# Kernel tuning notes

Hardware: AMD Instinct MI355X
Metric: run time of the kernel (lower is better)

The kernel has to match this reference:

```python
import jax, jax.numpy as jnp
import numpy as np

B, F, D, C, K = 131072, 32, 16, 64, 8  # batch, features, qsvt degree, classes, KAN grid
CLIP = 1.0 - 1e-6


def setup_inputs() -> dict:
    key = jax.random.key(0)
    ks = jax.random.split(key, 7)
    return {
        "X": jax.random.normal(ks[0], (B, F), jnp.float32),
        "qsvt_phases": 0.1 * jax.random.normal(ks[1], (D,), jnp.float32),
        "lcu_weights": jax.random.uniform(ks[2], (F, D), jnp.float32),
        "sum_scale": jnp.ones((F,), jnp.float32) + 0.1 * jax.random.normal(ks[3], (F,), jnp.float32),
        "sum_bias": 0.1 * jax.random.normal(ks[4], (F,), jnp.float32),
        "kan_coeff": jax.random.normal(ks[5], (C, F, K), jnp.float32) / np.sqrt(F * K),
        "kan_bias": jnp.zeros((C,), jnp.float32),
    }


def reference(X, qsvt_phases, lcu_weights, sum_scale, sum_bias, kan_coeff, kan_bias):
    # QSVT: Chebyshev-with-phases polynomial features of each scalar input,
    # vectorized over (batch, feature) instead of the original Python loops.
    degree = qsvt_phases.shape[0]
    grid = kan_coeff.shape[-1]
    theta = jnp.arccos(jnp.clip(X, -CLIP, CLIP))                  # [B,F]
    kd = jnp.arange(1, degree + 1, dtype=X.dtype)                 # [D]
    qsvt_vecs = jnp.cos(theta[..., None] * kd + qsvt_phases)      # [B,F,D]
    # LCU block: normalized linear combination over the degree axis -> scalar per (b,f)
    lcu = jnp.sum(qsvt_vecs * lcu_weights, axis=-1) / (
        jnp.sum(jnp.abs(lcu_weights), axis=-1) + 1e-6)            # [B,F]
    # QuantumSumBlock (one per feature): per-feature affine + tanh squash
    feat = jnp.tanh(sum_scale * lcu + sum_bias)                   # [B,F]
    # KAN layer: Chebyshev basis expansion then per-(class,feature,basis) coefficients
    t2 = jnp.arccos(jnp.clip(feat, -CLIP, CLIP))                  # [B,F]
    kk = jnp.arange(grid, dtype=X.dtype)                          # [K]
    basis = jnp.cos(t2[..., None] * kk)                           # [B,F,K]
    return jnp.einsum('bfk,cfk->bc', basis, kan_coeff) + kan_bias  # [B,C]
```

## Files before the change

kernel.cpp:

```cpp
#include <hip/hip_runtime.h>
#include <hip/hip_bf16.h>

#define F 32
#define Dd 16
#define C 64
#define Kk 8
#define CLIPV (1.0f - 1e-6f)
#define K2 2.8853900817779268f
#define NBLK 1024
#define MT 2

typedef short v8s __attribute__((ext_vector_type(8)));
typedef float v4f __attribute__((ext_vector_type(4)));
typedef float v2f __attribute__((ext_vector_type(2)));

static __device__ inline unsigned pkbf(float lo, float hi) {
    const unsigned l = __bfloat16_as_ushort(__float2bfloat16(lo));
    const unsigned hh = __bfloat16_as_ushort(__float2bfloat16(hi));
    return l | (hh << 16);
}

#define BAR_WRITES() do {                                        \
    asm volatile("s_waitcnt lgkmcnt(0)" ::: "memory");           \
    __builtin_amdgcn_s_barrier();                                \
    asm volatile("" ::: "memory");                               \
} while (0)
#define BAR_READS() do {                                         \
    asm volatile("" ::: "memory");                               \
    __builtin_amdgcn_s_barrier();                                \
    asm volatile("" ::: "memory");                               \
} while (0)

__global__ __launch_bounds__(256, 4) void qkan_kernel(
    const float* __restrict__ X,
    const float* __restrict__ phases,
    const float* __restrict__ lcu_w,
    const float* __restrict__ sscale,
    const float* __restrict__ sbias,
    const float* __restrict__ coeff,
    const float* __restrict__ kbias,
    float* __restrict__ out)
{
    __shared__ unsigned short s_basis[F * 512];

    const int tid = threadIdx.x;
    const int lane = tid & 63;
    const int wu = __builtin_amdgcn_readfirstlane(tid >> 6);
    const int h = lane >> 4;
    const int r16 = lane & 15;
    const int fe = tid & 31;
    const int fe7 = fe & 7;
    const int rg = tid >> 5;

    const int rb0 = blockIdx.x * (MT * 64);

    float xq[8];
    {
        const float* xp = X + (size_t)(rb0 + rg * 8) * F + fe;
#pragma unroll
        for (int m = 0; m < 8; ++m) xq[m] = xp[m * F];
    }

    v2f cc[16];
    float fbias;
    {
        const float* lwf = lcu_w + fe * Dd;
        float wv[16];
        float asum = 0.f;
#pragma unroll
        for (int d = 0; d < Dd; ++d) {
            wv[d] = lwf[d];
            asum += fabsf(wv[d]);
        }
        const float sc = K2 * sscale[fe] / (asum + 1e-6f);
#pragma unroll
        for (int d = 0; d < Dd; ++d) {
            float sp, cp;
            __sincosf(phases[d], &sp, &cp);
            cc[d][0] = sc * wv[d] * cp;
            cc[d][1] = -sc * wv[d] * sp;
        }
        fbias = K2 * sbias[fe];
    }

    v8s Bfr[8];
    const int cidx = wu * 16 + r16;
#pragma unroll
    for (int q = 0; q < 8; ++q) {
        const float* gp = coeff + ((size_t)(cidx * F + 4 * q + h) * Kk);
        const float4 g0 = *reinterpret_cast<const float4*>(gp);
        const float4 g1 = *reinterpret_cast<const float4*>(gp + 4);
        union { unsigned u[4]; v8s v; } bb;
        bb.u[0] = pkbf(g0.x, g0.y);
        bb.u[1] = pkbf(g0.z, g0.w);
        bb.u[2] = pkbf(g1.x, g1.y);
        bb.u[3] = pkbf(g1.z, g1.w);
        Bfr[q] = bb.v;
    }
    const float biasreg = kbias[cidx];

    for (int mt = 0; mt < MT; ++mt) {
        const int row_base = rb0 + mt * 64;
        if (mt) BAR_READS();

        float xn[8];
        if (mt + 1 < MT) {
            const float* xp = X + (size_t)(row_base + 64 + rg * 8) * F + fe;
#pragma unroll
            for (int m = 0; m < 8; ++m) xn[m] = xp[m * F];
        }

#pragma unroll
        for (int m = 0; m < 8; ++m) {
            const float x = __builtin_amdgcn_fmed3f(xq[m], -CLIPV, CLIPV);
            const float s1 = __builtin_amdgcn_sqrtf(__builtin_fmaf(-x, x, 1.f));
            const float tx = x + x;
            const v2f tx2 = {tx, tx};
            v2f w = {0.f, 0.f}, wp = {0.f, 0.f};
#pragma unroll
            for (int j = 15; j >= 0; --j) {
                const v2f wn = __builtin_elementwise_fma(tx2, w, cc[j] - wp);
                wp = w;
                w = wn;
            }
            float z = fbias - wp[0];
            z = __builtin_fmaf(x, w[0], z);
            z = __builtin_fmaf(s1, w[1], z);
            const float e = __builtin_amdgcn_exp2f(z);
            const float rr = __builtin_amdgcn_rcpf(e + 1.f);
            const float t = __builtin_fmaf(-2.f, rr, 1.f);
            const float t2 = t + t;
            const float b1 = t;
            const float b2 = t2 * b1 - 1.f;
            const float b3 = t2 * b2 - b1;
            const float b4 = t2 * b3 - b2;
            const float b5 = t2 * b4 - b3;
            const float b6 = t2 * b5 - b4;
            const float b7 = t2 * b6 - b5;
            uint4 pk;
            pk.x = pkbf(1.f, b1);
            pk.y = pkbf(b2, b3);
            pk.z = pkbf(b4, b5);
            pk.w = pkbf(b6, b7);
            *reinterpret_cast<uint4*>(
                &s_basis[fe * 512 + rg * 64 + ((m ^ fe7) << 3)]) = pk;
        }
        BAR_WRITES();

#pragma unroll
        for (int t = 0; t < 4; ++t) {
            const int s0 = ((t * 16 + r16) ^ h) << 3;
            v4f acc = {biasreg, biasreg, biasreg, biasreg};
#pragma unroll
            for (int q = 0; q < 8; ++q) {
                const int idx = (4 * q + h) * 512 + (s0 ^ ((q & 1) << 5));
                const v8s a = *reinterpret_cast<const v8s*>(&s_basis[idx]);
                acc = __builtin_amdgcn_mfma_f32_16x16x32_bf16(a, Bfr[q], acc, 0, 0, 0);
            }
            const int row0 = row_base + t * 16 + h * 4;
#pragma unroll
            for (int i = 0; i < 4; ++i) {
                out[(size_t)(row0 + i) * C + cidx] = acc[i];
            }
        }

        if (mt + 1 < MT) {
#pragma unroll
            for (int m = 0; m < 8; ++m) xq[m] = xn[m];
        }
    }
}

extern "C" void kernel_launch(void* const* d_in, const int* in_sizes, int n_in,
                              void* d_out, int out_size, void* d_ws, size_t ws_size,
                              hipStream_t stream) {
    const float* X  = (const float*)d_in[0];
    const float* ph = (const float*)d_in[1];
    const float* lw = (const float*)d_in[2];
    const float* ss = (const float*)d_in[3];
    const float* sb = (const float*)d_in[4];
    const float* kc = (const float*)d_in[5];
    const float* kb = (const float*)d_in[6];
    float* out = (float*)d_out;
    qkan_kernel<<<dim3(NBLK), dim3(256), 0, stream>>>(X, ph, lw, ss, sb, kc, kb, out);
}
```

Baseline: 25.84 us.

## Switch KAN matmul to 32x32x16 MFMA with per-wave row/column tiling

Replaces the per-wave 16x16x32 bf16 MFMA loop, where each wave covered 16 classes over all 64 rows in four tiles, with 32x32x16 MFMA. Each wave now owns a 32-row by 32-class tile and loads 16 coefficient fragments instead of 8. The intent is fewer MFMA issues and LDS reads per output element and better operand reuse. In exchange it uses more registers for B fragments and accumulators, and drops the occupancy hint in launch_bounds, which may lower occupancy.

```diff
diff --git a/kernel.cpp b/kernel.cpp
--- a/kernel.cpp
+++ b/kernel.cpp
@@ -11,7 +11,7 @@
 #define MT 2
 
 typedef short v8s __attribute__((ext_vector_type(8)));
-typedef float v4f __attribute__((ext_vector_type(4)));
+typedef float v16f __attribute__((ext_vector_type(16)));
 typedef float v2f __attribute__((ext_vector_type(2)));
 
 static __device__ inline unsigned pkbf(float lo, float hi) {
@@ -31,7 +31,7 @@
     asm volatile("" ::: "memory");                               \
 } while (0)
 
-__global__ __launch_bounds__(256, 4) void qkan_kernel(
+__global__ __launch_bounds__(256) void qkan_kernel(
     const float* __restrict__ X,
     const float* __restrict__ phases,
     const float* __restrict__ lcu_w,
@@ -46,11 +46,14 @@
     const int tid = threadIdx.x;
     const int lane = tid & 63;
     const int wu = __builtin_amdgcn_readfirstlane(tid >> 6);
-    const int h = lane >> 4;
-    const int r16 = lane & 15;
+    const int hh = lane >> 5;
+    const int l31 = lane & 31;
     const int fe = tid & 31;
     const int fe7 = fe & 7;
     const int rg = tid >> 5;
+
+    const int rh = wu >> 1;
+    const int ct = wu & 1;
 
     const int rb0 = blockIdx.x * (MT * 64);
 
@@ -83,11 +86,11 @@
         fbias = K2 * sbias[fe];
     }
 
-    v8s Bfr[8];
-    const int cidx = wu * 16 + r16;
+    v8s Bfr[16];
+    const int cidx = ct * 32 + l31;
 #pragma unroll
-    for (int q = 0; q < 8; ++q) {
-        const float* gp = coeff + ((size_t)(cidx * F + 4 * q + h) * Kk);
+    for (int q = 0; q < 16; ++q) {
+        const float* gp = coeff + ((size_t)(cidx * F + 2 * q + hh) * Kk);
         const float4 g0 = *reinterpret_cast<const float4*>(gp);
         const float4 g1 = *reinterpret_cast<const float4*>(gp + 4);
         union { unsigned u[4]; v8s v; } bb;
@@ -147,20 +150,23 @@
         }
         BAR_WRITES();
 
+        {
+            v16f acc;
 #pragma unroll
-        for (int t = 0; t < 4; ++t) {
-            const int s0 = ((t * 16 + r16) ^ h) << 3;
-            v4f acc = {biasreg, biasreg, biasreg, biasreg};
+            for (int r = 0; r < 16; ++r) acc[r] = biasreg;
 #pragma unroll
-            for (int q = 0; q < 8; ++q) {
-                const int idx = (4 * q + h) * 512 + (s0 ^ ((q & 1) << 5));
-                const v8s a = *reinterpret_cast<const v8s*>(&s_basis[idx]);
-                acc = __builtin_amdgcn_mfma_f32_16x16x32_bf16(a, Bfr[q], acc, 0, 0, 0);
+            for (int q = 0; q < 16; ++q) {
+                const int f = 2 * q + hh;
+                const int slot = (rh * 32 + l31) ^ (f & 7);
+                const v8s a = *reinterpret_cast<const v8s*>(
+                    &s_basis[f * 512 + slot * 8]);
+                acc = __builtin_amdgcn_mfma_f32_32x32x16_bf16(a, Bfr[q], acc, 0, 0, 0);
             }
-            const int row0 = row_base + t * 16 + h * 4;
+            const int row00 = row_base + rh * 32 + 4 * hh;
 #pragma unroll
-            for (int i = 0; i < 4; ++i) {
-                out[(size_t)(row0 + i) * C + cidx] = acc[i];
+            for (int r = 0; r < 16; ++r) {
+                const int rrow = (r & 3) + 8 * (r >> 2);
+                out[(size_t)(row00 + rrow) * C + cidx] = acc[r];
             }
         }
 
```

Measured after the change: 34.84 us. 1.35x slower.
